# Optimization experiments

Measured on AMD Instinct MI355X. Metric: run time of the kernel, lower is better.

## Reference

```python
import jax, jax.numpy as jnp
import numpy as np

IN_DIM, ATT_DIM, OUT_DIM, NH = 1024, 64, 64, 16
ATT_BIAS = 0.5


def setup_inputs() -> dict:
    key = jax.random.key(0)
    ks = jax.random.split(key, 11)
    B, S = 2, 2048
    s_in = 1.0 / np.sqrt(IN_DIM)
    s_o = 1.0 / np.sqrt(NH * OUT_DIM)
    return {
        "q": jax.random.normal(ks[0], (B, S, IN_DIM), jnp.float32),
        "k": jax.random.normal(ks[1], (B, S, IN_DIM), jnp.float32),
        "v": jax.random.normal(ks[2], (B, S, IN_DIM), jnp.float32),
        "Wq": jax.random.uniform(ks[3], (IN_DIM, NH * ATT_DIM), jnp.float32, -s_in, s_in),
        "bq": jax.random.uniform(ks[4], (NH * ATT_DIM,), jnp.float32, -s_in, s_in),
        "Wk": jax.random.uniform(ks[5], (IN_DIM, NH * ATT_DIM), jnp.float32, -s_in, s_in),
        "bk": jax.random.uniform(ks[6], (NH * ATT_DIM,), jnp.float32, -s_in, s_in),
        "Wv": jax.random.uniform(ks[7], (IN_DIM, NH * OUT_DIM), jnp.float32, -s_in, s_in),
        "bv": jax.random.uniform(ks[8], (NH * OUT_DIM,), jnp.float32, -s_in, s_in),
        "Wo": jax.random.uniform(ks[9], (NH * OUT_DIM, OUT_DIM), jnp.float32, -s_o, s_o),
        "bo": jax.random.uniform(ks[10], (OUT_DIM,), jnp.float32, -s_o, s_o),
    }


def reference(q, k, v, Wq, bq, Wk, bk, Wv, bv, Wo, bo):
    B, S, _ = q.shape
    scale = ATT_DIM ** -0.5
    # projections -> [B, H, S, d]
    qh = (q @ Wq + bq).reshape(B, S, NH, ATT_DIM).transpose(0, 2, 1, 3)
    kh = (k @ Wk + bk).reshape(B, S, NH, ATT_DIM).transpose(0, 2, 1, 3)
    vh = (v @ Wv + bv).reshape(B, S, NH, OUT_DIM).transpose(0, 2, 1, 3)
    # sigmoid-biased scores then softmax over keys
    scores = jnp.einsum("bhqd,bhkd->bhqk", qh * scale, kh)
    scores = jax.nn.sigmoid(scores) - ATT_BIAS
    attn = jax.nn.softmax(scores, axis=-1)
    out = jnp.einsum("bhqk,bhkd->bhqd", attn, vh)  # dropout p=0 -> identity
    out = out.transpose(0, 2, 1, 3).reshape(B, S, NH * OUT_DIM)
    return out @ Wo + bo
```

## Files before the change

kernel.cpp:

```cpp
#include <hip/hip_runtime.h>
#include <hip/hip_bf16.h>
#include <stdint.h>

typedef __bf16 bf16x8 __attribute__((ext_vector_type(8)));
typedef float  f32x4  __attribute__((ext_vector_type(4)));
typedef short  short4v __attribute__((ext_vector_type(4)));

__device__ __forceinline__ unsigned short f2bf(float f) {
  union { float f; unsigned u; } x; x.f = f;
  unsigned r = x.u + 0x7fffu + ((x.u >> 16) & 1u);
  return (unsigned short)(r >> 16);
}

__device__ __forceinline__ unsigned pack_rne(float a, float b) {
  unsigned ua = __float_as_uint(a), ub = __float_as_uint(b);
  ua = ua + 0x7fffu + ((ua >> 16) & 1u);
  ub = ub + 0x7fffu + ((ub >> 16) & 1u);
  return __builtin_amdgcn_perm(ub, ua, 0x07060302);
}

__device__ __forceinline__ f32x4 mfma16(short4v a, short4v b, f32x4 c) {
#if __has_builtin(__builtin_amdgcn_mfma_f32_16x16x16bf16_1k)
  return __builtin_amdgcn_mfma_f32_16x16x16bf16_1k(a, b, c, 0, 0, 0);
#else
  f32x4 d;
  asm volatile("v_mfma_f32_16x16x16_bf16 %0, %1, %2, %3\n\ts_nop 7\n\ts_nop 7"
               : "=v"(d) : "v"(a), "v"(b), "v"(c));
  return d;
#endif
}

__device__ __forceinline__ float fast_exp2(float p) {
#if __has_builtin(__builtin_amdgcn_exp2f)
  return __builtin_amdgcn_exp2f(p);
#else
  return exp2f(p);
#endif
}

__device__ __forceinline__ void gll16(const void* g, void* l) {
  __builtin_amdgcn_global_load_lds((const __attribute__((address_space(1))) void*)g,
                                   (__attribute__((address_space(3))) void*)l, 16, 0, 0);
}

__global__ __launch_bounds__(256) void k_prep(
    const float* __restrict__ q, const float* __restrict__ k, const float* __restrict__ v,
    const float* __restrict__ Wq, const float* __restrict__ Wk,
    const float* __restrict__ Wv, const float* __restrict__ Wo,
    const float* __restrict__ bo,
    unsigned short* __restrict__ qb, unsigned short* __restrict__ kb,
    unsigned short* __restrict__ vb,
    unsigned short* __restrict__ Wqt, unsigned short* __restrict__ Wkt,
    unsigned short* __restrict__ Wvt, unsigned short* __restrict__ Wot,
    float* __restrict__ out) {
  __shared__ float tt[32][33];
  int b = blockIdx.x, tid = threadIdx.x;
  if (b < 12288) {
    int z = b >> 12;
    const float* src = z == 0 ? q : z == 1 ? k : v;
    unsigned short* dst = z == 0 ? qb : z == 1 ? kb : vb;
    size_t i = (size_t)(b & 4095) * 256 + tid;
    float4 f = ((const float4*)src)[i];
    ushort4 o;
    o.x = f2bf(f.x); o.y = f2bf(f.y); o.z = f2bf(f.z); o.w = f2bf(f.w);
    ((ushort4*)dst)[i] = o;
  } else if (b < 15424) {
    int t = b - 12288;
    const float* W; unsigned short* Wt; int C, c0, r0;
    if (t < 3072) {
      int z = t >> 10;
      W = z == 0 ? Wq : z == 1 ? Wk : Wv;
      Wt = z == 0 ? Wqt : z == 1 ? Wkt : Wvt;
      C = 1024; int tile = t & 1023;
      c0 = (tile & 31) * 32; r0 = (tile >> 5) * 32;
    } else {
      int t2 = t - 3072;
      W = Wo; Wt = Wot; C = 64;
      c0 = (t2 & 1) * 32; r0 = (t2 >> 1) * 32;
    }
    int tx = tid & 31, ty = tid >> 5;
    #pragma unroll
    for (int i = 0; i < 32; i += 8)
      tt[ty + i][tx] = W[(size_t)(r0 + ty + i) * C + c0 + tx];
    __syncthreads();
    #pragma unroll
    for (int i = 0; i < 32; i += 8)
      Wt[(size_t)(c0 + ty + i) * 1024 + r0 + tx] = f2bf(tt[tx][ty + i]);
  } else {
    int t3 = b - 15424;
    int i = t3 * 1024 + tid * 4;
    float4 bv4 = *(const float4*)(bo + (i & 63));
    *(float4*)(out + i) = bv4;
  }
}

__global__ __launch_bounds__(256, 3) void k_proj(
    const unsigned short* __restrict__ qb, const unsigned short* __restrict__ kb,
    const unsigned short* __restrict__ vb,
    const unsigned short* __restrict__ Wqt, const unsigned short* __restrict__ Wkt,
    const unsigned short* __restrict__ Wvt,
    const float* __restrict__ bq, const float* __restrict__ bk, const float* __restrict__ bv,
    unsigned short* __restrict__ qh, unsigned short* __restrict__ kh,
    unsigned short* __restrict__ vht) {
  int z = blockIdx.z;
  const unsigned short* A  = z == 0 ? qb  : z == 1 ? kb  : vb;
  const unsigned short* Bt = z == 0 ? Wqt : z == 1 ? Wkt : Wvt;
  const float* bias = z == 0 ? bq : z == 1 ? bk : bv;

  int m0 = blockIdx.y * 128;
  int n0 = blockIdx.x * 128;

  __shared__ __attribute__((aligned(16))) unsigned short As[128 * 64];
  __shared__ __attribute__((aligned(16))) unsigned short Bs[128 * 64];

  int tid = threadIdx.x;
  int w = tid >> 6, lane = tid & 63;
  int wm = w >> 1, wn = w & 1;
  int lr = lane & 15, lk = lane >> 4;

  f32x4 acc[4][4] = {};

  for (int k0 = 0; k0 < 1024; k0 += 64) {
    #pragma unroll
    for (int i = 0; i < 4; ++i) {
      int cc = i * 256 + tid;
      int r = cc >> 3;
      int j = (cc & 7) ^ (r & 7);
      gll16(A + (size_t)(m0 + r) * 1024 + k0 + j * 8, As + (size_t)(i * 256 + w * 64) * 8);
    }
    #pragma unroll
    for (int i = 0; i < 4; ++i) {
      int cc = i * 256 + tid;
      int r = cc >> 3;
      int j = (cc & 7) ^ (r & 7);
      gll16(Bt + (size_t)(n0 + r) * 1024 + k0 + j * 8, Bs + (size_t)(i * 256 + w * 64) * 8);
    }
    __syncthreads();
    #pragma unroll
    for (int ks = 0; ks < 2; ++ks) {
      bf16x8 af[4], bfr[4];
      #pragma unroll
      for (int mt = 0; mt < 4; ++mt) {
        int r = wm * 64 + mt * 16 + lr;
        af[mt] = *(const bf16x8*)(As + r * 64 + ((ks * 4 + lk) ^ (r & 7)) * 8);
      }
      #pragma unroll
      for (int nt = 0; nt < 4; ++nt) {
        int r = wn * 64 + nt * 16 + lr;
        bfr[nt] = *(const bf16x8*)(Bs + r * 64 + ((ks * 4 + lk) ^ (r & 7)) * 8);
      }
      #pragma unroll
      for (int mt = 0; mt < 4; ++mt)
        #pragma unroll
        for (int nt = 0; nt < 4; ++nt)
          acc[mt][nt] = __builtin_amdgcn_mfma_f32_16x16x32_bf16(af[mt], bfr[nt], acc[mt][nt], 0, 0, 0);
    }
    __syncthreads();
  }

  #pragma unroll
  for (int nt = 0; nt < 4; ++nt) {
    int n = n0 + wn * 64 + nt * 16 + lr;
    float bv_ = bias[n];
    int h = n >> 6, d = n & 63;
    #pragma unroll
    for (int mt = 0; mt < 4; ++mt) {
      int mbase = m0 + wm * 64 + mt * 16 + lk * 4;
      int b = mbase >> 11, s = mbase & 2047;
      if (z == 2) {
        size_t o = ((size_t)(b * 16 + h) * 64 + d) * 2048 + s;
        ushort4 pk;
        pk.x = f2bf(acc[mt][nt][0] + bv_);
        pk.y = f2bf(acc[mt][nt][1] + bv_);
        pk.z = f2bf(acc[mt][nt][2] + bv_);
        pk.w = f2bf(acc[mt][nt][3] + bv_);
        *(ushort4*)(vht + o) = pk;
      } else {
        unsigned short* dst = (z == 0) ? qh : kh;
        float sc = (z == 0) ? 0.125f : 1.0f;
        #pragma unroll
        for (int rg = 0; rg < 4; ++rg) {
          float val = (acc[mt][nt][rg] + bv_) * sc;
          float pv = __shfl_xor(val, 1, 64);
          if ((lr & 1) == 0) {
            unsigned pkv = pack_rne(val, pv);
            *(unsigned*)(dst + ((size_t)(b * 16 + h) * 2048 + (s + rg)) * 64 + d) = pkv;
          }
        }
      }
    }
  }
}

__global__ __launch_bounds__(256, 2) void k_attn(
    const unsigned short* __restrict__ qh, const unsigned short* __restrict__ kh,
    const unsigned short* __restrict__ vht, unsigned short* __restrict__ attout) {
  int bh = blockIdx.y;
  int q0 = blockIdx.x * 128;
  const unsigned short* Q = qh + (size_t)bh * 2048 * 64;
  const unsigned short* Kg = kh + (size_t)bh * 2048 * 64;
  const unsigned short* Vg = vht + (size_t)bh * 64 * 2048;

  __shared__ __attribute__((aligned(16))) unsigned short KV[17408];
  __shared__ float lsum[128];

  int tid = threadIdx.x;
  int w = tid >> 6, lane = tid & 63;
  int wm = w >> 1, wn = w & 1;
  int c = lane & 15, qd = lane >> 4;

  bf16x8 qf[4][2];
  #pragma unroll
  for (int nt = 0; nt < 4; ++nt)
    #pragma unroll
    for (int ks = 0; ks < 2; ++ks)
      qf[nt][ks] = *(const bf16x8*)(Q + (size_t)(q0 + wn * 64 + nt * 16 + c) * 64 + ks * 32 + qd * 8);

  size_t kOff[2], vOff[2]; int lOff[2];
  #pragma unroll
  for (int i = 0; i < 2; ++i) {
    int cc = i * 256 + w * 64 + lane;
    int r = cc >> 3;
    int j = (cc & 7) ^ (r & 7);
    kOff[i] = (size_t)r * 64 + j * 8;
    vOff[i] = (size_t)r * 2048 + j * 8;
    lOff[i] = (i * 256 + w * 64) * 8;
  }

  #pragma unroll
  for (int i = 0; i < 2; ++i) {
    gll16(Kg + kOff[i], KV + lOff[i]);
    gll16(Vg + vOff[i], KV + 4096 + lOff[i]);
  }
  Kg += 4096; Vg += 64;

  int kfA[2][2], vfA[4][2];
  #pragma unroll
  for (int mt = 0; mt < 2; ++mt) {
    int r = wm * 32 + mt * 16 + c;
    #pragma unroll
    for (int ks = 0; ks < 2; ++ks)
      kfA[mt][ks] = r * 64 + ((ks * 4 + qd) ^ (r & 7)) * 8;
  }
  #pragma unroll
  for (int dt = 0; dt < 4; ++dt) {
    int r = dt * 16 + c;
    #pragma unroll
    for (int mt = 0; mt < 2; ++mt)
      vfA[dt][mt] = r * 64 + ((4 * wm + 2 * mt + (qd >> 1)) ^ (r & 7)) * 8 + (qd & 1) * 4;
  }

  const short one_bf = (short)0x3F80;
  short4v ones = {one_bf, one_bf, one_bf, one_bf};

  __syncthreads();

  f32x4 o[4][4] = {};
  f32x4 qacc[4] = {};

  for (int kt = 0; kt < 32; ++kt) {
    unsigned short* Kc = KV + (kt & 1) * 8192;
    unsigned short* Vc = Kc + 4096;
    if (kt + 1 < 32) {
      unsigned short* Kn = KV + ((kt & 1) ^ 1) * 8192;
      #pragma unroll
      for (int i = 0; i < 2; ++i) {
        gll16(Kg + kOff[i], Kn + lOff[i]);
        gll16(Vg + vOff[i], Kn + 4096 + lOff[i]);
      }
      Kg += 4096; Vg += 64;
    }

    f32x4 s[2][4] = {};
    #pragma unroll
    for (int ks = 0; ks < 2; ++ks) {
      bf16x8 kf[2];
      #pragma unroll
      for (int mt = 0; mt < 2; ++mt)
        kf[mt] = *(const bf16x8*)(Kc + kfA[mt][ks]);
      #pragma unroll
      for (int mt = 0; mt < 2; ++mt)
        #pragma unroll
        for (int nt = 0; nt < 4; ++nt)
          s[mt][nt] = __builtin_amdgcn_mfma_f32_16x16x32_bf16(kf[mt], qf[nt][ks], s[mt][nt], 0, 0, 0);
    }

    unsigned pk[2][4][2];
    #pragma unroll
    for (int mt = 0; mt < 2; ++mt)
      #pragma unroll
      for (int nt = 0; nt < 4; ++nt) {
        unsigned wu[4];
        #pragma unroll
        for (int rg = 0; rg < 4; ++rg) {
          float sv = __builtin_amdgcn_fmed3f(s[mt][nt][rg], -4.0f, 4.0f);
          float z = sv * sv;
          float p = fmaf(z, fmaf(z, fmaf(z, -3.9242863e-5f, 1.5674414e-3f),
                                  -2.6566200e-2f), 3.5838444e-1f) * sv;
          wu[rg] = __float_as_uint(fast_exp2(p));
        }
        pk[mt][nt][0] = __builtin_amdgcn_perm(wu[1], wu[0], 0x07060302);
        pk[mt][nt][1] = __builtin_amdgcn_perm(wu[3], wu[2], 0x07060302);
      }

    short4v vfr[4][2];
    #pragma unroll
    for (int dt = 0; dt < 4; ++dt)
      #pragma unroll
      for (int mt = 0; mt < 2; ++mt)
        vfr[dt][mt] = *(const short4v*)(Vc + vfA[dt][mt]);
    #pragma unroll
    for (int nt = 0; nt < 4; ++nt)
      #pragma unroll
      for (int mt = 0; mt < 2; ++mt) {
        union { unsigned u[2]; short4v s4; } bb;
        bb.u[0] = pk[mt][nt][0];
        bb.u[1] = pk[mt][nt][1];
        qacc[nt] = mfma16(ones, bb.s4, qacc[nt]);
        #pragma unroll
        for (int dt = 0; dt < 4; ++dt)
          o[dt][nt] = mfma16(vfr[dt][mt], bb.s4, o[dt][nt]);
      }
    __syncthreads();
  }

  float* Ored = (float*)KV;
  if (wm == 1) {
    #pragma unroll
    for (int nt = 0; nt < 4; ++nt) {
      int ql = wn * 64 + nt * 16 + c;
      #pragma unroll
      for (int dt = 0; dt < 4; ++dt)
        *(f32x4*)(Ored + ql * 68 + dt * 16 + qd * 4) = o[dt][nt];
      if (qd == 0) lsum[ql] = qacc[nt][0];
    }
  }
  __syncthreads();
  if (wm == 0) {
    int b = bh >> 4, h = bh & 15;
    #pragma unroll
    for (int nt = 0; nt < 4; ++nt) {
      int ql = wn * 64 + nt * 16 + c;
      float inv = __builtin_amdgcn_rcpf(qacc[nt][0] + lsum[ql]);
      size_t rowoff = ((size_t)(b * 2048 + q0 + ql)) * 1024 + h * 64;
      #pragma unroll
      for (int dt = 0; dt < 4; ++dt) {
        f32x4 r = *(const f32x4*)(Ored + ql * 68 + dt * 16 + qd * 4);
        f32x4 t = o[dt][nt];
        uint2 pko;
        pko.x = pack_rne((t[0] + r[0]) * inv, (t[1] + r[1]) * inv);
        pko.y = pack_rne((t[2] + r[2]) * inv, (t[3] + r[3]) * inv);
        *(uint2*)(attout + rowoff + dt * 16 + qd * 4) = pko;
      }
    }
  }
}

__global__ __launch_bounds__(256) void k_oproj(
    const unsigned short* __restrict__ attout, const unsigned short* __restrict__ Wot,
    float* __restrict__ out) {
  int m0 = blockIdx.x * 64;
  int kbase = blockIdx.y * 256;
  __shared__ __attribute__((aligned(16))) unsigned short As[64 * 32];
  __shared__ __attribute__((aligned(16))) unsigned short Bs[64 * 32];
  int tid = threadIdx.x;
  int w = tid >> 6, lane = tid & 63;
  int lr = lane & 15, lk = lane >> 4;

  f32x4 acc[4] = {};

  for (int k0 = kbase; k0 < kbase + 256; k0 += 32) {
    {
      int cc = tid;
      int r = cc >> 2;
      int j = (cc & 3) ^ ((r >> 1) & 3);
      gll16(attout + (size_t)(m0 + r) * 1024 + k0 + j * 8, As + (size_t)(w * 64) * 8);
      gll16(Wot + (size_t)r * 1024 + k0 + j * 8, Bs + (size_t)(w * 64) * 8);
    }
    __syncthreads();
    bf16x8 af, bfr[4];
    {
      int r = w * 16 + lr;
      af = *(const bf16x8*)(As + r * 32 + ((lk ^ ((r >> 1) & 3))) * 8);
    }
    #pragma unroll
    for (int nt = 0; nt < 4; ++nt) {
      int r = nt * 16 + lr;
      bfr[nt] = *(const bf16x8*)(Bs + r * 32 + ((lk ^ ((r >> 1) & 3))) * 8);
    }
    #pragma unroll
    for (int nt = 0; nt < 4; ++nt)
      acc[nt] = __builtin_amdgcn_mfma_f32_16x16x32_bf16(af, bfr[nt], acc[nt], 0, 0, 0);
    __syncthreads();
  }
  #pragma unroll
  for (int nt = 0; nt < 4; ++nt) {
    int n = nt * 16 + lr;
    #pragma unroll
    for (int rg = 0; rg < 4; ++rg) {
      int m = m0 + w * 16 + lk * 4 + rg;
      atomicAdd(&out[(size_t)m * 64 + n], acc[nt][rg]);
    }
  }
}

extern "C" void kernel_launch(void* const* d_in, const int* in_sizes, int n_in,
                              void* d_out, int out_size, void* d_ws, size_t ws_size,
                              hipStream_t stream) {
  const float* q  = (const float*)d_in[0];
  const float* k  = (const float*)d_in[1];
  const float* v  = (const float*)d_in[2];
  const float* Wq = (const float*)d_in[3];
  const float* bq = (const float*)d_in[4];
  const float* Wk = (const float*)d_in[5];
  const float* bk = (const float*)d_in[6];
  const float* Wv = (const float*)d_in[7];
  const float* bv = (const float*)d_in[8];
  const float* Wo = (const float*)d_in[9];
  const float* bo = (const float*)d_in[10];
  float* out = (float*)d_out;

  char* ws = (char*)d_ws;
  const size_t MB = 1024 * 1024;
  unsigned short* qb  = (unsigned short*)(ws + 0 * MB);
  unsigned short* kb  = (unsigned short*)(ws + 8 * MB);
  unsigned short* vb  = (unsigned short*)(ws + 16 * MB);
  unsigned short* Wqt = (unsigned short*)(ws + 24 * MB);
  unsigned short* Wkt = (unsigned short*)(ws + 26 * MB);
  unsigned short* Wvt = (unsigned short*)(ws + 28 * MB);
  unsigned short* Wot = (unsigned short*)(ws + 30 * MB);
  unsigned short* qh  = (unsigned short*)(ws + 32 * MB);
  unsigned short* kh  = (unsigned short*)(ws + 40 * MB);
  unsigned short* vht = (unsigned short*)(ws + 48 * MB);
  unsigned short* att = (unsigned short*)(ws + 56 * MB);

  k_prep<<<dim3(15680), dim3(256), 0, stream>>>(q, k, v, Wq, Wk, Wv, Wo, bo,
                                                qb, kb, vb, Wqt, Wkt, Wvt, Wot, out);
  k_proj<<<dim3(8, 32, 3), dim3(256), 0, stream>>>(qb, kb, vb, Wqt, Wkt, Wvt,
                                                   bq, bk, bv, qh, kh, vht);
  k_attn<<<dim3(16, 32), dim3(256), 0, stream>>>(qh, kh, vht, att);
  k_oproj<<<dim3(64, 4), dim3(256), 0, stream>>>(att, Wot, out);
}
```

Measured before the change: 219.4 us.

## Fuse output projection into attention epilogue with per-head atomic accumulation

The separate output-projection kernel is removed and each attention block now multiplies its normalized per-head output tile by that head's slice of Wo with MFMA in the epilogue. Results are accumulated into the final output with atomicAdd. This avoids writing and re-reading the bf16 attention buffer and saves a kernel launch. In exchange there are 16 heads contributing atomics per output element instead of 4 K-splits, which raises atomic traffic and contention. Extra registers are also held in the attention epilogue.

```diff
diff --git a/kernel.cpp b/kernel.cpp
--- a/kernel.cpp
+++ b/kernel.cpp
@@ -194,7 +194,8 @@
 
 __global__ __launch_bounds__(256, 2) void k_attn(
     const unsigned short* __restrict__ qh, const unsigned short* __restrict__ kh,
-    const unsigned short* __restrict__ vht, unsigned short* __restrict__ attout) {
+    const unsigned short* __restrict__ vht, const unsigned short* __restrict__ Wot,
+    float* __restrict__ out) {
   int bh = blockIdx.y;
   int q0 = blockIdx.x * 128;
   const unsigned short* Q = qh + (size_t)bh * 2048 * 64;
@@ -338,68 +339,44 @@
   __syncthreads();
   if (wm == 0) {
     int b = bh >> 4, h = bh & 15;
+
+    short4v wa[4][4];
+    #pragma unroll
+    for (int mt = 0; mt < 4; ++mt)
+      #pragma unroll
+      for (int dt = 0; dt < 4; ++dt)
+        wa[mt][dt] = *(const short4v*)(Wot + (size_t)(mt * 16 + c) * 1024 +
+                                       h * 64 + dt * 16 + qd * 4);
+
+    f32x4 oc[4][4] = {};
     #pragma unroll
     for (int nt = 0; nt < 4; ++nt) {
       int ql = wn * 64 + nt * 16 + c;
       float inv = __builtin_amdgcn_rcpf(qacc[nt][0] + lsum[ql]);
-      size_t rowoff = ((size_t)(b * 2048 + q0 + ql)) * 1024 + h * 64;
       #pragma unroll
       for (int dt = 0; dt < 4; ++dt) {
         f32x4 r = *(const f32x4*)(Ored + ql * 68 + dt * 16 + qd * 4);
         f32x4 t = o[dt][nt];
-        uint2 pko;
-        pko.x = pack_rne((t[0] + r[0]) * inv, (t[1] + r[1]) * inv);
-        pko.y = pack_rne((t[2] + r[2]) * inv, (t[3] + r[3]) * inv);
-        *(uint2*)(attout + rowoff + dt * 16 + qd * 4) = pko;
-      }
-    }
-  }
-}
-
-__global__ __launch_bounds__(256) void k_oproj(
-    const unsigned short* __restrict__ attout, const unsigned short* __restrict__ Wot,
-    float* __restrict__ out) {
-  int m0 = blockIdx.x * 64;
-  int kbase = blockIdx.y * 256;
-  __shared__ __attribute__((aligned(16))) unsigned short As[64 * 32];
-  __shared__ __attribute__((aligned(16))) unsigned short Bs[64 * 32];
-  int tid = threadIdx.x;
-  int w = tid >> 6, lane = tid & 63;
-  int lr = lane & 15, lk = lane >> 4;
-
-  f32x4 acc[4] = {};
-
-  for (int k0 = kbase; k0 < kbase + 256; k0 += 32) {
-    {
-      int cc = tid;
-      int r = cc >> 2;
-      int j = (cc & 3) ^ ((r >> 1) & 3);
-      gll16(attout + (size_t)(m0 + r) * 1024 + k0 + j * 8, As + (size_t)(w * 64) * 8);
-      gll16(Wot + (size_t)r * 1024 + k0 + j * 8, Bs + (size_t)(w * 64) * 8);
-    }
-    __syncthreads();
-    bf16x8 af, bfr[4];
-    {
-      int r = w * 16 + lr;
-      af = *(const bf16x8*)(As + r * 32 + ((lk ^ ((r >> 1) & 3))) * 8);
-    }
+        union { unsigned u[2]; short4v s4; } bb;
+        bb.u[0] = pack_rne((t[0] + r[0]) * inv, (t[1] + r[1]) * inv);
+        bb.u[1] = pack_rne((t[2] + r[2]) * inv, (t[3] + r[3]) * inv);
+        #pragma unroll
+        for (int mt = 0; mt < 4; ++mt)
+          oc[mt][nt] = mfma16(wa[mt][dt], bb.s4, oc[mt][nt]);
+      }
+    }
+
     #pragma unroll
     for (int nt = 0; nt < 4; ++nt) {
-      int r = nt * 16 + lr;
-      bfr[nt] = *(const bf16x8*)(Bs + r * 32 + ((lk ^ ((r >> 1) & 3))) * 8);
-    }
-    #pragma unroll
-    for (int nt = 0; nt < 4; ++nt)
-      acc[nt] = __builtin_amdgcn_mfma_f32_16x16x32_bf16(af, bfr[nt], acc[nt], 0, 0, 0);
-    __syncthreads();
-  }
-  #pragma unroll
-  for (int nt = 0; nt < 4; ++nt) {
-    int n = nt * 16 + lr;
-    #pragma unroll
-    for (int rg = 0; rg < 4; ++rg) {
-      int m = m0 + w * 16 + lk * 4 + rg;
-      atomicAdd(&out[(size_t)m * 64 + n], acc[nt][rg]);
+      int qg = q0 + wn * 64 + nt * 16 + c;
+      size_t rowoff = (size_t)(b * 2048 + qg) * 64;
+      #pragma unroll
+      for (int mt = 0; mt < 4; ++mt) {
+        int dout = mt * 16 + qd * 4;
+        #pragma unroll
+        for (int rg = 0; rg < 4; ++rg)
+          atomicAdd(&out[rowoff + dout + rg], oc[mt][nt][rg]);
+      }
     }
   }
 }
@@ -432,12 +409,10 @@
   unsigned short* qh  = (unsigned short*)(ws + 32 * MB);
   unsigned short* kh  = (unsigned short*)(ws + 40 * MB);
   unsigned short* vht = (unsigned short*)(ws + 48 * MB);
-  unsigned short* att = (unsigned short*)(ws + 56 * MB);
 
   k_prep<<<dim3(15680), dim3(256), 0, stream>>>(q, k, v, Wq, Wk, Wv, Wo, bo,
                                                 qb, kb, vb, Wqt, Wkt, Wvt, Wot, out);
   k_proj<<<dim3(8, 32, 3), dim3(256), 0, stream>>>(qb, kb, vb, Wqt, Wkt, Wvt,
                                                    bq, bk, bv, qh, kh, vht);
-  k_attn<<<dim3(16, 32), dim3(256), 0, stream>>>(qh, kh, vht, att);
-  k_oproj<<<dim3(64, 4), dim3(256), 0, stream>>>(att, Wot, out);
-}
+  k_attn<<<dim3(16, 32), dim3(256), 0, stream>>>(qh, kh, vht, Wot, out);
+}
```

Result: slower. 278.4 us (+26.8%).
